# Optimization experiments

Measured on AMD Instinct MI355X. Metric: run time of the kernel, lower is better.

## Reference

```python
import math
import jax, jax.numpy as jnp
from jax import lax
import numpy as np

N, C, H, W = 32, 256, 56, 56

def setup_inputs() -> dict:
    key = jax.random.key(0)
    k = jax.random.split(key, 5)
    return {
        "x": jax.random.normal(k[0], (N, C, H, W), dtype=jnp.float32),
        "p1_w": jax.random.normal(k[1], (H, W, C, 1), dtype=jnp.float32) * 0.1,
        "conv_w": jax.random.normal(k[2], (C, C // 2, 3, 3), dtype=jnp.float32) * 0.05,
        "p4_w": jax.random.normal(k[3], (1, C, C), dtype=jnp.float32) * 0.1,
        "p5_w": jax.random.normal(k[4], (C, 1), dtype=jnp.float32) * 0.1,
    }

def reference(x, p1_w, conv_w, p4_w, p5_w):
    n, c, h, w = x.shape
    inv_sqrt_c = 1.0 / math.sqrt(c)
    # t_1: einsum 'abcd,cdef->abef' -> [n, c, c, 1] -> [n, c, c]
    t1 = jnp.einsum('nchw,hwef->ncef', x, p1_w)[..., 0]
    # t_3: grouped 3x3 conv, groups=2, no bias -> [n, c, h, w]
    t3 = lax.conv_general_dilated(
        x, conv_w, window_strides=(1, 1), padding=((1, 1), (1, 1)),
        dimension_numbers=('NCHW', 'OIHW', 'NCHW'), feature_group_count=2)
    # t_4: broadcast elementwise scale [1,c,c] * [n,c,c]
    t4 = p4_w * t1
    # t_5: [n,c,c] @ [c,1] -> [n,c]
    t5 = jnp.einsum('nab,bo->nao', t4, p5_w)[..., 0]
    # t_6: bmm(t4 [n,c,c], t3 [n,c,hw]) / sqrt(c) -> [n,c,h,w]
    t6 = (jnp.einsum('nab,nbs->nas', t4, t3.reshape(n, c, h * w))
          .reshape(n, c, h, w)) * inv_sqrt_c
    # t_7: bmm(t5 [n,1,c], x [n,c,hw]) / sqrt(c) -> [n,h,w]
    t7 = (jnp.einsum('nc,ncs->ns', t5, x.reshape(n, c, h * w))
          .reshape(n, h, w)) * inv_sqrt_c
    # t_8: broadcast add [n,1,h,w] + [n,c,h,w]
    return t7[:, None, :, :] + t6
```

## Files before the change

### kernel.cpp

```cpp
#include <hip/hip_runtime.h>

#define HWB   3136
#define HWPAD 3200
#define SPAD  3364

typedef __attribute__((ext_vector_type(8))) short bf16x8;
typedef __attribute__((ext_vector_type(4))) float f32x4;

__device__ __forceinline__ unsigned short f2bf(float f) {
    unsigned u = __float_as_uint(f);
    unsigned r = (u + 0x7fffu + ((u >> 16) & 1u)) >> 16;
    return (unsigned short)r;
}
__device__ __forceinline__ float bf2f(unsigned short h) {
    return __uint_as_float(((unsigned)h) << 16);
}
__device__ __forceinline__ void gl_lds16(const void* g, void* l) {
    __builtin_amdgcn_global_load_lds(
        (const __attribute__((address_space(1))) void*)g,
        (__attribute__((address_space(3))) void*)l, 16, 0, 0);
}

__global__ __launch_bounds__(256) void k_prep(
    const float* __restrict__ x, unsigned short* __restrict__ xc,
    unsigned short* __restrict__ xp,
    const float* __restrict__ p1, const float* __restrict__ cw,
    unsigned short* __restrict__ p1t, unsigned short* __restrict__ wp)
{
    const int b = blockIdx.x, t = threadIdx.x;
    if (b < 6272) {
        __shared__ unsigned tile[64 * 33];
        const int n = b / 196, rem = b - n * 196;
        const int c0 = (rem / 49) * 64, s0 = (rem % 49) * 64;
        const int cp = t >> 3;
        const int sg = (t & 7) * 8;

        const float* src = x + ((size_t)(n * 256 + c0 + 2 * cp)) * HWB + s0 + sg;
        unsigned short b0[8], b1[8];
        {
            float4 v0 = *(const float4*)(src);
            float4 v1 = *(const float4*)(src + 4);
            float4 w0 = *(const float4*)(src + HWB);
            float4 w1 = *(const float4*)(src + HWB + 4);
            b0[0] = f2bf(v0.x); b0[1] = f2bf(v0.y); b0[2] = f2bf(v0.z); b0[3] = f2bf(v0.w);
            b0[4] = f2bf(v1.x); b0[5] = f2bf(v1.y); b0[6] = f2bf(v1.z); b0[7] = f2bf(v1.w);
            b1[0] = f2bf(w0.x); b1[1] = f2bf(w0.y); b1[2] = f2bf(w0.z); b1[3] = f2bf(w0.w);
            b1[4] = f2bf(w1.x); b1[5] = f2bf(w1.y); b1[6] = f2bf(w1.z); b1[7] = f2bf(w1.w);
        }
        unsigned short* xcb = xc + ((size_t)(n * 256 + c0 + 2 * cp)) * HWB + s0 + sg;
        *(bf16x8*)xcb = *(const bf16x8*)&b0[0];
        *(bf16x8*)(xcb + HWB) = *(const bf16x8*)&b1[0];
#pragma unroll
        for (int k = 0; k < 8; ++k)
            tile[(sg + k) * 33 + cp] = (unsigned)b0[k] | ((unsigned)b1[k] << 16);
        __syncthreads();
        const int r = t >> 2;
        const int cq = (t & 3) * 8;
        unsigned d[8];
#pragma unroll
        for (int j = 0; j < 8; ++j)
            d[j] = tile[r * 33 + cq + j];
        const int s = s0 + r;
        const int sp = s + 2 * (s / 56) + 59;
        unsigned* dst = (unsigned*)(xp + ((size_t)n * SPAD + sp) * 256 + c0 + 2 * cq);
        *(uint4*)dst = make_uint4(d[0], d[1], d[2], d[3]);
        *(uint4*)(dst + 4) = make_uint4(d[4], d[5], d[6], d[7]);
    } else if (b < 7056) {
        __shared__ unsigned short tile[32][33];
        const int b2 = b - 6272;
        const int h0 = (b2 % 98) * 32, e0 = (b2 / 98) * 32;
        const int lx = t & 31, ly = t >> 5;
#pragma unroll
        for (int it = 0; it < 4; ++it) {
            int lh = ly + it * 8;
            tile[lh][lx] = f2bf(p1[(size_t)(h0 + lh) * 256 + e0 + lx]);
        }
        __syncthreads();
#pragma unroll
        for (int it = 0; it < 4; ++it) {
            int le = ly + it * 8;
            p1t[(size_t)(e0 + le) * HWB + h0 + lx] = tile[lx][le];
        }
    } else if (b < 7312) {
        const int o = b - 7056;
#pragma unroll
        for (int k = t; k < 1152; k += 256) {
            int tap = k >> 7, ci = k & 127;
            wp[(size_t)o * 1152 + k] = f2bf(cw[(size_t)o * 1152 + ci * 9 + tap]);
        }
    } else {
        const int bb = b - 7312;
        const int n = bb / 29, xb = bb - n * 29;
        const int idx = xb * 256 + t;
        if (idx < 228 * 32) {
            const int i = idx >> 5, ch = idx & 31;
            int sp;
            if (i < 58)       sp = i;
            else if (i < 116) sp = 3306 + (i - 58);
            else if (i < 172) sp = (i - 115) * 58;
            else              sp = (i - 171) * 58 + 57;
            bf16x8 z = {};
            *(bf16x8*)&xp[((size_t)n * SPAD + sp) * 256 + ch * 8] = z;
        }
    }
}

__global__ __launch_bounds__(256) void k_mfma(
    const unsigned short* __restrict__ xp, const unsigned short* __restrict__ wp,
    unsigned short* __restrict__ t3cl,
    const unsigned short* __restrict__ xc, const unsigned short* __restrict__ p1t,
    float* __restrict__ part)
{
    __shared__ short As[2][128 * 64];
    __shared__ short Bs[2][128 * 64];
    const int tid = threadIdx.x;
    const int wave = tid >> 6, lane = tid & 63;
    const int wm = (wave >> 1) * 64, wn = (wave & 1) * 64;
    const int rl = tid >> 3, q = tid & 7;
    const int swq = (q ^ (rl & 7)) * 8;
    const int ldst = rl * 64 + q * 8;
    const int frow = lane & 15, quad = lane >> 4, sw = frow & 7;

    if (blockIdx.x < 1600) {
        const int orig = blockIdx.x;
        const int wgid = (orig & 7) * 200 + (orig >> 3);
        const int ng = wgid / 25;
        const int tileS = (wgid - ng * 25) * 128;
        const int n = ng >> 1, g = ng & 1;

        const unsigned short* xpn = xp + (size_t)n * SPAD * 256 + g * 128 + swq;
        const unsigned short* arow[4];
        const unsigned short* brow[4];
#pragma unroll
        for (int p = 0; p < 4; ++p) {
            int s = tileS + p * 32 + rl;
            int sc = s < HWB ? s : HWB - 1;
            int sp = sc + 2 * (sc / 56) + 59;
            arow[p] = xpn + (size_t)sp * 256;
            brow[p] = wp + (size_t)(g * 128 + p * 32 + rl) * 1152 + swq;
        }

        f32x4 acc[4][4] = {};
        int rofA[4], rofB[4];
#pragma unroll
        for (int i = 0; i < 4; ++i) {
            rofA[i] = (wm + i * 16 + frow) * 64;
            rofB[i] = (wn + i * 16 + frow) * 64;
        }
        {
            const int shift0 = (-59) * 256;
#pragma unroll
            for (int p = 0; p < 4; ++p) {
                gl_lds16(arow[p] + shift0, &As[0][p * 2048 + ldst]);
                gl_lds16(brow[p], &Bs[0][p * 2048 + ldst]);
            }
        }
        __syncthreads();

        int cur = 0;
#pragma unroll
        for (int t = 0; t < 18; ++t) {
            if (t < 17) {
                const int tn = t + 1;
                const int tap = tn >> 1;
                const int shift = ((tap / 3 - 1) * 58 + (tap % 3 - 1)) * 256 + (tn & 1) * 64;
#pragma unroll
                for (int p = 0; p < 4; ++p) {
                    gl_lds16(arow[p] + shift, &As[cur ^ 1][p * 2048 + ldst]);
                    gl_lds16(brow[p] + tn * 64, &Bs[cur ^ 1][p * 2048 + ldst]);
                }
            }
            const short* Ab = As[cur];
            const short* Bb = Bs[cur];
#pragma unroll
            for (int h = 0; h < 2; ++h) {
                bf16x8 af[4], bfr[4];
#pragma unroll
                for (int i = 0; i < 4; ++i)
                    af[i] = *(const bf16x8*)&Ab[rofA[i] + ((h * 4 + quad) ^ sw) * 8];
#pragma unroll
                for (int j = 0; j < 4; ++j)
                    bfr[j] = *(const bf16x8*)&Bb[rofB[j] + ((h * 4 + quad) ^ sw) * 8];
#pragma unroll
                for (int i = 0; i < 4; ++i)
#pragma unroll
                    for (int j = 0; j < 4; ++j)
                        acc[i][j] = __builtin_amdgcn_mfma_f32_16x16x32_bf16(af[i], bfr[j], acc[i][j], 0, 0, 0);
            }
            __syncthreads();
            cur ^= 1;
        }
        unsigned short* ob = t3cl + (size_t)n * HWPAD * 256 + g * 128;
#pragma unroll
        for (int i = 0; i < 4; ++i)
#pragma unroll
            for (int r = 0; r < 4; ++r) {
                int s = tileS + wm + i * 16 + quad * 4 + r;
                int c = wn + frow;
#pragma unroll
                for (int j = 0; j < 4; ++j) {
                    float v = (s < HWB) ? acc[i][j][r] : 0.f;
                    ob[(size_t)s * 256 + c + j * 16] = f2bf(v);
                }
            }
    } else {
        const int orig = blockIdx.x - 1600;
        const int wgid = (orig & 7) * 32 + (orig >> 3);
        const int z = wgid >> 7;
        const int rem = wgid & 127;
        const int tileM = (rem >> 1) * 128;
        const int tileN = (rem & 1) * 128;
        const int kbase = z * 1600;
        const int nk = z ? 24 : 25;

        const unsigned short* asrc = xc + (size_t)(tileM + rl) * HWB + kbase + swq;
        const unsigned short* bsrc = p1t + (size_t)(tileN + rl) * HWB + kbase + swq;

        f32x4 acc[4][4] = {};
#pragma unroll
        for (int p = 0; p < 4; ++p) {
            gl_lds16(asrc + (size_t)(p * 32) * HWB, &As[0][p * 2048 + ldst]);
            gl_lds16(bsrc + (size_t)(p * 32) * HWB, &Bs[0][p * 2048 + ldst]);
        }
        __syncthreads();

        int cur = 0;
        for (int i2 = 0; i2 < nk; ++i2) {
            if (i2 + 1 < nk) {
                const int kn = (i2 + 1) * 64;
#pragma unroll
                for (int p = 0; p < 4; ++p) {
                    gl_lds16(asrc + (size_t)(p * 32) * HWB + kn, &As[cur ^ 1][p * 2048 + ldst]);
                    gl_lds16(bsrc + (size_t)(p * 32) * HWB + kn, &Bs[cur ^ 1][p * 2048 + ldst]);
                }
            }
            const short* Ab = As[cur];
            const short* Bb = Bs[cur];
#pragma unroll
            for (int h = 0; h < 2; ++h) {
                bf16x8 af[4], bfr[4];
#pragma unroll
                for (int i = 0; i < 4; ++i)
                    af[i] = *(const bf16x8*)&Ab[(wm + i * 16 + frow) * 64 + ((h * 4 + quad) ^ sw) * 8];
#pragma unroll
                for (int j = 0; j < 4; ++j)
                    bfr[j] = *(const bf16x8*)&Bb[(wn + j * 16 + frow) * 64 + ((h * 4 + quad) ^ sw) * 8];
#pragma unroll
                for (int i = 0; i < 4; ++i)
#pragma unroll
                    for (int j = 0; j < 4; ++j)
                        acc[i][j] = __builtin_amdgcn_mfma_f32_16x16x32_bf16(af[i], bfr[j], acc[i][j], 0, 0, 0);
            }
            __syncthreads();
            cur ^= 1;
        }
        float* ob = part + (size_t)z * 8192 * 256;
#pragma unroll
        for (int j = 0; j < 4; ++j) {
            const int e = tileN + wn + j * 16 + frow;
#pragma unroll
            for (int i = 0; i < 4; ++i)
#pragma unroll
                for (int r = 0; r < 4; ++r) {
                    int m = tileM + wm + i * 16 + quad * 4 + r;
                    ob[(size_t)m * 256 + e] = acc[i][j][r];
                }
        }
    }
}

__global__ __launch_bounds__(256) void k_t4scale(
    const float* __restrict__ part, const float* __restrict__ p4,
    const float* __restrict__ p5, unsigned short* __restrict__ t4h,
    float* __restrict__ t5)
{
    const int row = blockIdx.x * 4 + (threadIdx.x >> 6);
    const int lane = threadIdx.x & 63;
    const size_t off = (size_t)row * 256 + lane * 4;
    const size_t slab = (size_t)8192 * 256;
    float4 a0 = *(const float4*)&part[off];
    float4 a1 = *(const float4*)&part[off + slab];
    float4 a;
    a.x = a0.x + a1.x; a.y = a0.y + a1.y; a.z = a0.z + a1.z; a.w = a0.w + a1.w;
    float4 sc = *(const float4*)&p4[(size_t)(row & 255) * 256 + lane * 4];
    float4 pv = *(const float4*)&p5[lane * 4];
    float v0 = a.x * sc.x, v1 = a.y * sc.y, v2 = a.z * sc.z, v3 = a.w * sc.w;
    ushort4 o;
    o.x = f2bf(v0); o.y = f2bf(v1); o.z = f2bf(v2); o.w = f2bf(v3);
    *(ushort4*)&t4h[(size_t)row * 256 + lane * 4] = o;
    float sum = v0 * pv.x + v1 * pv.y + v2 * pv.z + v3 * pv.w;
#pragma unroll
    for (int offd = 32; offd > 0; offd >>= 1) sum += __shfl_down(sum, offd);
    if (lane == 0) t5[row] = sum;
}

__global__ __launch_bounds__(256) void k_bmm(
    const unsigned short* __restrict__ t4h, const unsigned short* __restrict__ t3cl,
    const unsigned short* __restrict__ xp, const float* __restrict__ t5,
    float* __restrict__ out)
{
    __shared__ short As[2][128 * 64];
    __shared__ short Bs[2][128 * 64];
    __shared__ float t5s[256];
    __shared__ float t7loc[128];
    const int tid = threadIdx.x;
    const int orig = blockIdx.x;
    const int wgid = (orig & 7) * 200 + (orig >> 3);
    const int n = wgid / 50;
    const int rem = wgid - n * 50;
    const int tileA = (rem / 25) * 128;
    const int tileS = (rem % 25) * 128;
    const int wave = tid >> 6, lane = tid & 63;
    const int wm = (wave >> 1) * 64, wn = (wave & 1) * 64;

    const int rl = tid >> 3, q = tid & 7;
    const int swq = (q ^ (rl & 7)) * 8;
    const unsigned short* asrc = t4h + ((size_t)n * 256 + tileA + rl) * 256 + swq;
    const unsigned short* bsrc = t3cl + ((size_t)n * HWPAD + tileS + rl) * 256 + swq;

    f32x4 acc[4][4] = {};
    const int frow = lane & 15, quad = lane >> 4, sw = frow & 7;
    const int ldst = rl * 64 + q * 8;

    t5s[tid] = t5[n * 256 + tid];
#pragma unroll
    for (int p = 0; p < 4; ++p) {
        gl_lds16(asrc + (size_t)(p * 32) * 256, &As[0][p * 2048 + ldst]);
        gl_lds16(bsrc + (size_t)(p * 32) * 256, &Bs[0][p * 2048 + ldst]);
    }
    __syncthreads();

    if (tid < 128) {
        const int s = tileS + tid;
        float accv = 0.f;
        if (s < HWB) {
            const int sp = s + 2 * (s / 56) + 59;
            const unsigned short* row = xp + ((size_t)n * SPAD + sp) * 256;
#pragma unroll
            for (int j = 0; j < 32; ++j) {
                bf16x8 v = *(const bf16x8*)(row + j * 8);
#pragma unroll
                for (int k = 0; k < 8; ++k)
                    accv += t5s[j * 8 + k] * bf2f((unsigned short)v[k]);
            }
        }
        t7loc[tid] = accv * 0.0625f;
    }

    int cur = 0;
#pragma unroll
    for (int k0 = 0; k0 < 256; k0 += 64) {
        if (k0 < 192) {
            const int kn = k0 + 64;
#pragma unroll
            for (int p = 0; p < 4; ++p) {
                gl_lds16(asrc + (size_t)(p * 32) * 256 + kn, &As[cur ^ 1][p * 2048 + ldst]);
                gl_lds16(bsrc + (size_t)(p * 32) * 256 + kn, &Bs[cur ^ 1][p * 2048 + ldst]);
            }
        }
        const short* Ab = As[cur];
        const short* Bb = Bs[cur];
#pragma unroll
        for (int h = 0; h < 2; ++h) {
            bf16x8 af[4], bfr[4];
#pragma unroll
            for (int i = 0; i < 4; ++i)
                af[i] = *(const bf16x8*)&Ab[(wm + i * 16 + frow) * 64 + ((h * 4 + quad) ^ sw) * 8];
#pragma unroll
            for (int j = 0; j < 4; ++j)
                bfr[j] = *(const bf16x8*)&Bb[(wn + j * 16 + frow) * 64 + ((h * 4 + quad) ^ sw) * 8];
#pragma unroll
            for (int i = 0; i < 4; ++i)
#pragma unroll
                for (int j = 0; j < 4; ++j)
                    acc[i][j] = __builtin_amdgcn_mfma_f32_16x16x32_bf16(af[i], bfr[j], acc[i][j], 0, 0, 0);
        }
        __syncthreads();
        cur ^= 1;
    }
    float* ob = out + (size_t)n * 256 * HWB;
#pragma unroll
    for (int j = 0; j < 4; ++j) {
        const int sLoc = wn + j * 16 + frow;
        const int s = tileS + sLoc;
        if (s >= HWB) continue;
        const float t7v = t7loc[sLoc];
#pragma unroll
        for (int i = 0; i < 4; ++i)
#pragma unroll
            for (int r = 0; r < 4; ++r) {
                int a = tileA + wm + i * 16 + quad * 4 + r;
                ob[(size_t)a * HWB + s] = acc[i][j][r] * 0.0625f + t7v;
            }
    }
}

extern "C" void kernel_launch(void* const* d_in, const int* in_sizes, int n_in,
                              void* d_out, int out_size, void* d_ws, size_t ws_size,
                              hipStream_t stream) {
    const float* x  = (const float*)d_in[0];
    const float* p1 = (const float*)d_in[1];
    const float* cw = (const float*)d_in[2];
    const float* p4 = (const float*)d_in[3];
    const float* p5 = (const float*)d_in[4];

    char* w = (char*)d_ws;
    unsigned short* xp    = (unsigned short*)w;  w += (size_t)32 * SPAD * 256 * 2;
    unsigned short* t3cl  = (unsigned short*)w;  w += (size_t)32 * HWPAD * 256 * 2;
    unsigned short* p1t   = (unsigned short*)w;  w += (size_t)256 * HWB * 2;
    unsigned short* wpack = (unsigned short*)w;  w += (size_t)256 * 1152 * 2;
    unsigned short* t4h   = (unsigned short*)w;  w += (size_t)8192 * 256 * 2;
    float* t5             = (float*)w;           w += (size_t)8192 * 4;

    char* o = (char*)d_out;
    unsigned short* xc = (unsigned short*)o;
    float* part        = (float*)(o + (size_t)32 * 256 * HWB * 2);
    float* out = (float*)d_out;

    k_prep    <<<dim3(8240),  256, 0, stream>>>(x, xc, xp, p1, cw, p1t, wpack);
    k_mfma    <<<dim3(1856),  256, 0, stream>>>(xp, wpack, t3cl, xc, p1t, part);
    k_t4scale <<<dim3(2048),  256, 0, stream>>>(part, p4, p5, t4h, t5);
    k_bmm     <<<dim3(1600),  256, 0, stream>>>(t4h, t3cl, xp, t5, out);
}
```

Before: 329.9 us.

## Fuse grouped conv into bmm kernel, keeping t3 tile in LDS

The grouped 3x3 conv is moved out of the combined MFMA kernel and fused into the final bmm kernel. Each block computes a 64-pixel by 256-channel conv tile for both groups, packs it to bf16 in LDS, and immediately multiplies by t4 (read directly from global), so the t3 intermediate is never written to or read back from HBM. The gemm1 part becomes its own small 256-block kernel. In exchange the bmm stage has smaller spatial tiles, reads t4 fragments from global without LDS staging, and carries more register pressure, which may lower occupancy. The gemm1 kernel also no longer overlaps with the conv work.

```diff
diff --git a/kernel.cpp b/kernel.cpp
--- a/kernel.cpp
+++ b/kernel.cpp
@@ -1,7 +1,6 @@
 #include <hip/hip_runtime.h>
 
 #define HWB   3136
-#define HWPAD 3200
 #define SPAD  3364
 
 typedef __attribute__((ext_vector_type(8))) short bf16x8;
@@ -105,167 +104,81 @@
     }
 }
 
-__global__ __launch_bounds__(256) void k_mfma(
-    const unsigned short* __restrict__ xp, const unsigned short* __restrict__ wp,
-    unsigned short* __restrict__ t3cl,
+__global__ __launch_bounds__(256) void k_gemm1(
     const unsigned short* __restrict__ xc, const unsigned short* __restrict__ p1t,
     float* __restrict__ part)
 {
     __shared__ short As[2][128 * 64];
     __shared__ short Bs[2][128 * 64];
     const int tid = threadIdx.x;
+    const int orig = blockIdx.x;
+    const int wgid = (orig & 7) * 32 + (orig >> 3);
+    const int z = wgid >> 7;
+    const int rem = wgid & 127;
+    const int tileM = (rem >> 1) * 128;
+    const int tileN = (rem & 1) * 128;
+    const int kbase = z * 1600;
+    const int nk = z ? 24 : 25;
     const int wave = tid >> 6, lane = tid & 63;
     const int wm = (wave >> 1) * 64, wn = (wave & 1) * 64;
+
     const int rl = tid >> 3, q = tid & 7;
     const int swq = (q ^ (rl & 7)) * 8;
+    const unsigned short* asrc = xc + (size_t)(tileM + rl) * HWB + kbase + swq;
+    const unsigned short* bsrc = p1t + (size_t)(tileN + rl) * HWB + kbase + swq;
+
+    f32x4 acc[4][4] = {};
+    const int frow = lane & 15, quad = lane >> 4, sw = frow & 7;
     const int ldst = rl * 64 + q * 8;
-    const int frow = lane & 15, quad = lane >> 4, sw = frow & 7;
-
-    if (blockIdx.x < 1600) {
-        const int orig = blockIdx.x;
-        const int wgid = (orig & 7) * 200 + (orig >> 3);
-        const int ng = wgid / 25;
-        const int tileS = (wgid - ng * 25) * 128;
-        const int n = ng >> 1, g = ng & 1;
-
-        const unsigned short* xpn = xp + (size_t)n * SPAD * 256 + g * 128 + swq;
-        const unsigned short* arow[4];
-        const unsigned short* brow[4];
-#pragma unroll
-        for (int p = 0; p < 4; ++p) {
-            int s = tileS + p * 32 + rl;
-            int sc = s < HWB ? s : HWB - 1;
-            int sp = sc + 2 * (sc / 56) + 59;
-            arow[p] = xpn + (size_t)sp * 256;
-            brow[p] = wp + (size_t)(g * 128 + p * 32 + rl) * 1152 + swq;
-        }
-
-        f32x4 acc[4][4] = {};
-        int rofA[4], rofB[4];
-#pragma unroll
-        for (int i = 0; i < 4; ++i) {
-            rofA[i] = (wm + i * 16 + frow) * 64;
-            rofB[i] = (wn + i * 16 + frow) * 64;
-        }
-        {
-            const int shift0 = (-59) * 256;
+
+#pragma unroll
+    for (int p = 0; p < 4; ++p) {
+        gl_lds16(asrc + (size_t)(p * 32) * HWB, &As[0][p * 2048 + ldst]);
+        gl_lds16(bsrc + (size_t)(p * 32) * HWB, &Bs[0][p * 2048 + ldst]);
+    }
+    __syncthreads();
+
+    int cur = 0;
+    for (int i2 = 0; i2 < nk; ++i2) {
+        if (i2 + 1 < nk) {
+            const int kn = (i2 + 1) * 64;
 #pragma unroll
             for (int p = 0; p < 4; ++p) {
-                gl_lds16(arow[p] + shift0, &As[0][p * 2048 + ldst]);
-                gl_lds16(brow[p], &Bs[0][p * 2048 + ldst]);
-            }
+                gl_lds16(asrc + (size_t)(p * 32) * HWB + kn, &As[cur ^ 1][p * 2048 + ldst]);
+                gl_lds16(bsrc + (size_t)(p * 32) * HWB + kn, &Bs[cur ^ 1][p * 2048 + ldst]);
+            }
+        }
+        const short* Ab = As[cur];
+        const short* Bb = Bs[cur];
+#pragma unroll
+        for (int h = 0; h < 2; ++h) {
+            bf16x8 af[4], bfr[4];
+#pragma unroll
+            for (int i = 0; i < 4; ++i)
+                af[i] = *(const bf16x8*)&Ab[(wm + i * 16 + frow) * 64 + ((h * 4 + quad) ^ sw) * 8];
+#pragma unroll
+            for (int j = 0; j < 4; ++j)
+                bfr[j] = *(const bf16x8*)&Bb[(wn + j * 16 + frow) * 64 + ((h * 4 + quad) ^ sw) * 8];
+#pragma unroll
+            for (int i = 0; i < 4; ++i)
+#pragma unroll
+                for (int j = 0; j < 4; ++j)
+                    acc[i][j] = __builtin_amdgcn_mfma_f32_16x16x32_bf16(af[i], bfr[j], acc[i][j], 0, 0, 0);
         }
         __syncthreads();
-
-        int cur = 0;
-#pragma unroll
-        for (int t = 0; t < 18; ++t) {
-            if (t < 17) {
-                const int tn = t + 1;
-                const int tap = tn >> 1;
-                const int shift = ((tap / 3 - 1) * 58 + (tap % 3 - 1)) * 256 + (tn & 1) * 64;
-#pragma unroll
-                for (int p = 0; p < 4; ++p) {
-                    gl_lds16(arow[p] + shift, &As[cur ^ 1][p * 2048 + ldst]);
-                    gl_lds16(brow[p] + tn * 64, &Bs[cur ^ 1][p * 2048 + ldst]);
-                }
-            }
-            const short* Ab = As[cur];
-            const short* Bb = Bs[cur];
-#pragma unroll
-            for (int h = 0; h < 2; ++h) {
-                bf16x8 af[4], bfr[4];
-#pragma unroll
-                for (int i = 0; i < 4; ++i)
-                    af[i] = *(const bf16x8*)&Ab[rofA[i] + ((h * 4 + quad) ^ sw) * 8];
-#pragma unroll
-                for (int j = 0; j < 4; ++j)
-                    bfr[j] = *(const bf16x8*)&Bb[rofB[j] + ((h * 4 + quad) ^ sw) * 8];
-#pragma unroll
-                for (int i = 0; i < 4; ++i)
-#pragma unroll
-                    for (int j = 0; j < 4; ++j)
-                        acc[i][j] = __builtin_amdgcn_mfma_f32_16x16x32_bf16(af[i], bfr[j], acc[i][j], 0, 0, 0);
-            }
-            __syncthreads();
-            cur ^= 1;
-        }
-        unsigned short* ob = t3cl + (size_t)n * HWPAD * 256 + g * 128;
+        cur ^= 1;
+    }
+    float* ob = part + (size_t)z * 8192 * 256;
+#pragma unroll
+    for (int j = 0; j < 4; ++j) {
+        const int e = tileN + wn + j * 16 + frow;
 #pragma unroll
         for (int i = 0; i < 4; ++i)
 #pragma unroll
             for (int r = 0; r < 4; ++r) {
-                int s = tileS + wm + i * 16 + quad * 4 + r;
-                int c = wn + frow;
-#pragma unroll
-                for (int j = 0; j < 4; ++j) {
-                    float v = (s < HWB) ? acc[i][j][r] : 0.f;
-                    ob[(size_t)s * 256 + c + j * 16] = f2bf(v);
-                }
-            }
-    } else {
-        const int orig = blockIdx.x - 1600;
-        const int wgid = (orig & 7) * 32 + (orig >> 3);
-        const int z = wgid >> 7;
-        const int rem = wgid & 127;
-        const int tileM = (rem >> 1) * 128;
-        const int tileN = (rem & 1) * 128;
-        const int kbase = z * 1600;
-        const int nk = z ? 24 : 25;
-
-        const unsigned short* asrc = xc + (size_t)(tileM + rl) * HWB + kbase + swq;
-        const unsigned short* bsrc = p1t + (size_t)(tileN + rl) * HWB + kbase + swq;
-
-        f32x4 acc[4][4] = {};
-#pragma unroll
-        for (int p = 0; p < 4; ++p) {
-            gl_lds16(asrc + (size_t)(p * 32) * HWB, &As[0][p * 2048 + ldst]);
-            gl_lds16(bsrc + (size_t)(p * 32) * HWB, &Bs[0][p * 2048 + ldst]);
-        }
-        __syncthreads();
-
-        int cur = 0;
-        for (int i2 = 0; i2 < nk; ++i2) {
-            if (i2 + 1 < nk) {
-                const int kn = (i2 + 1) * 64;
-#pragma unroll
-                for (int p = 0; p < 4; ++p) {
-                    gl_lds16(asrc + (size_t)(p * 32) * HWB + kn, &As[cur ^ 1][p * 2048 + ldst]);
-                    gl_lds16(bsrc + (size_t)(p * 32) * HWB + kn, &Bs[cur ^ 1][p * 2048 + ldst]);
-                }
-            }
-            const short* Ab = As[cur];
-            const short* Bb = Bs[cur];
-#pragma unroll
-            for (int h = 0; h < 2; ++h) {
-                bf16x8 af[4], bfr[4];
-#pragma unroll
-                for (int i = 0; i < 4; ++i)
-                    af[i] = *(const bf16x8*)&Ab[(wm + i * 16 + frow) * 64 + ((h * 4 + quad) ^ sw) * 8];
-#pragma unroll
-                for (int j = 0; j < 4; ++j)
-                    bfr[j] = *(const bf16x8*)&Bb[(wn + j * 16 + frow) * 64 + ((h * 4 + quad) ^ sw) * 8];
-#pragma unroll
-                for (int i = 0; i < 4; ++i)
-#pragma unroll
-                    for (int j = 0; j < 4; ++j)
-                        acc[i][j] = __builtin_amdgcn_mfma_f32_16x16x32_bf16(af[i], bfr[j], acc[i][j], 0, 0, 0);
-            }
-            __syncthreads();
-            cur ^= 1;
-        }
-        float* ob = part + (size_t)z * 8192 * 256;
-#pragma unroll
-        for (int j = 0; j < 4; ++j) {
-            const int e = tileN + wn + j * 16 + frow;
-#pragma unroll
-            for (int i = 0; i < 4; ++i)
-#pragma unroll
-                for (int r = 0; r < 4; ++r) {
-                    int m = tileM + wm + i * 16 + quad * 4 + r;
-                    ob[(size_t)m * 256 + e] = acc[i][j][r];
-                }
-        }
+                int m = tileM + wm + i * 16 + quad * 4 + r;
+                ob[(size_t)m * 256 + e] = acc[i][j][r];
+            }
     }
 }
 
@@ -294,103 +207,174 @@
     if (lane == 0) t5[row] = sum;
 }
 
-__global__ __launch_bounds__(256) void k_bmm(
-    const unsigned short* __restrict__ t4h, const unsigned short* __restrict__ t3cl,
-    const unsigned short* __restrict__ xp, const float* __restrict__ t5,
+__global__ __launch_bounds__(256) void k_convbmm(
+    const unsigned short* __restrict__ xp, const unsigned short* __restrict__ wp,
+    const unsigned short* __restrict__ t4h, const float* __restrict__ t5,
     float* __restrict__ out)
 {
-    __shared__ short As[2][128 * 64];
-    __shared__ short Bs[2][128 * 64];
+    __shared__ short stg[24576];
     __shared__ float t5s[256];
-    __shared__ float t7loc[128];
+    __shared__ float t7loc[64];
     const int tid = threadIdx.x;
     const int orig = blockIdx.x;
-    const int wgid = (orig & 7) * 200 + (orig >> 3);
-    const int n = wgid / 50;
-    const int rem = wgid - n * 50;
-    const int tileA = (rem / 25) * 128;
-    const int tileS = (rem % 25) * 128;
+    const int wgid = (orig & 7) * 196 + (orig >> 3);
+    const int n = wgid / 49;
+    const int tileS = (wgid - n * 49) * 64;
     const int wave = tid >> 6, lane = tid & 63;
-    const int wm = (wave >> 1) * 64, wn = (wave & 1) * 64;
-
+    const int wm = (wave >> 1) * 32, wn = (wave & 1) * 64;
     const int rl = tid >> 3, q = tid & 7;
     const int swq = (q ^ (rl & 7)) * 8;
-    const unsigned short* asrc = t4h + ((size_t)n * 256 + tileA + rl) * 256 + swq;
-    const unsigned short* bsrc = t3cl + ((size_t)n * HWPAD + tileS + rl) * 256 + swq;
-
-    f32x4 acc[4][4] = {};
+    const int ldst = rl * 64 + q * 8;
     const int frow = lane & 15, quad = lane >> 4, sw = frow & 7;
-    const int ldst = rl * 64 + q * 8;
 
     t5s[tid] = t5[n * 256 + tid];
-#pragma unroll
-    for (int p = 0; p < 4; ++p) {
-        gl_lds16(asrc + (size_t)(p * 32) * 256, &As[0][p * 2048 + ldst]);
-        gl_lds16(bsrc + (size_t)(p * 32) * 256, &Bs[0][p * 2048 + ldst]);
+
+    int spA[2];
+#pragma unroll
+    for (int p = 0; p < 2; ++p) {
+        int s = tileS + p * 32 + rl;
+        spA[p] = s + 2 * (s / 56) + 59;
+    }
+
+    unsigned pk[2][4][2];
+    f32x4 acc[2][4];
+
+    for (int g = 0; g < 2; ++g) {
+        const unsigned short* xpn = xp + (size_t)n * SPAD * 256 + g * 128 + swq;
+        const unsigned short* arow[2];
+        const unsigned short* brow[4];
+#pragma unroll
+        for (int p = 0; p < 2; ++p) arow[p] = xpn + (size_t)spA[p] * 256;
+#pragma unroll
+        for (int p = 0; p < 4; ++p)
+            brow[p] = wp + (size_t)(g * 128 + p * 32 + rl) * 1152 + swq;
+#pragma unroll
+        for (int i = 0; i < 2; ++i)
+#pragma unroll
+            for (int j = 0; j < 4; ++j) acc[i][j] = (f32x4){0.f, 0.f, 0.f, 0.f};
+
+        {
+            const int shift0 = (-59) * 256;
+#pragma unroll
+            for (int p = 0; p < 2; ++p)
+                gl_lds16(arow[p] + shift0, &stg[p * 2048 + ldst]);
+#pragma unroll
+            for (int p = 0; p < 4; ++p)
+                gl_lds16(brow[p], &stg[8192 + p * 2048 + ldst]);
+        }
+        __syncthreads();
+
+        int cur = 0;
+#pragma unroll
+        for (int t = 0; t < 18; ++t) {
+            if (t < 17) {
+                const int tn = t + 1;
+                const int tap = tn >> 1;
+                const int shift = ((tap / 3 - 1) * 58 + (tap % 3 - 1)) * 256 + (tn & 1) * 64;
+#pragma unroll
+                for (int p = 0; p < 2; ++p)
+                    gl_lds16(arow[p] + shift, &stg[(cur ^ 1) * 4096 + p * 2048 + ldst]);
+#pragma unroll
+                for (int p = 0; p < 4; ++p)
+                    gl_lds16(brow[p] + tn * 64, &stg[8192 + (cur ^ 1) * 8192 + p * 2048 + ldst]);
+            }
+            const short* Ab = &stg[cur * 4096];
+            const short* Bb = &stg[8192 + cur * 8192];
+#pragma unroll
+            for (int h = 0; h < 2; ++h) {
+                bf16x8 af[2], bfr[4];
+#pragma unroll
+                for (int i = 0; i < 2; ++i)
+                    af[i] = *(const bf16x8*)&Ab[(wm + i * 16 + frow) * 64 + ((h * 4 + quad) ^ sw) * 8];
+#pragma unroll
+                for (int j = 0; j < 4; ++j)
+                    bfr[j] = *(const bf16x8*)&Bb[(wn + j * 16 + frow) * 64 + ((h * 4 + quad) ^ sw) * 8];
+#pragma unroll
+                for (int i = 0; i < 2; ++i)
+#pragma unroll
+                    for (int j = 0; j < 4; ++j)
+                        acc[i][j] = __builtin_amdgcn_mfma_f32_16x16x32_bf16(af[i], bfr[j], acc[i][j], 0, 0, 0);
+            }
+            __syncthreads();
+            cur ^= 1;
+        }
+        if (g == 0) {
+#pragma unroll
+            for (int i = 0; i < 2; ++i)
+#pragma unroll
+                for (int j = 0; j < 4; ++j) {
+                    pk[i][j][0] = (unsigned)f2bf(acc[i][j][0]) | ((unsigned)f2bf(acc[i][j][1]) << 16);
+                    pk[i][j][1] = (unsigned)f2bf(acc[i][j][2]) | ((unsigned)f2bf(acc[i][j][3]) << 16);
+                }
+        }
+    }
+
+#pragma unroll
+    for (int i = 0; i < 2; ++i)
+#pragma unroll
+        for (int r = 0; r < 4; ++r) {
+            const int sLoc = wm + i * 16 + quad * 4 + r;
+            const int key = sLoc & 7;
+#pragma unroll
+            for (int j = 0; j < 4; ++j) {
+                const int oc0 = wn + j * 16 + frow;
+                const unsigned short v0 = (unsigned short)(pk[i][j][r >> 1] >> ((r & 1) * 16));
+                stg[sLoc * 256 + (((oc0 >> 3) ^ key) << 3) + (oc0 & 7)] = (short)v0;
+                const int oc1 = 128 + oc0;
+                stg[sLoc * 256 + (((oc1 >> 3) ^ key) << 3) + (oc1 & 7)] = (short)f2bf(acc[i][j][r]);
+            }
+        }
+    if (tid < 64) {
+        const int s = tileS + tid;
+        const int sp = s + 2 * (s / 56) + 59;
+        const unsigned short* row = xp + ((size_t)n * SPAD + sp) * 256;
+        float accv = 0.f;
+#pragma unroll
+        for (int j = 0; j < 32; ++j) {
+            bf16x8 v = *(const bf16x8*)(row + j * 8);
+#pragma unroll
+            for (int k = 0; k < 8; ++k)
+                accv += t5s[j * 8 + k] * bf2f((unsigned short)v[k]);
+        }
+        t7loc[tid] = accv * 0.0625f;
     }
     __syncthreads();
 
-    if (tid < 128) {
-        const int s = tileS + tid;
-        float accv = 0.f;
-        if (s < HWB) {
-            const int sp = s + 2 * (s / 56) + 59;
-            const unsigned short* row = xp + ((size_t)n * SPAD + sp) * 256;
-#pragma unroll
-            for (int j = 0; j < 32; ++j) {
-                bf16x8 v = *(const bf16x8*)(row + j * 8);
-#pragma unroll
-                for (int k = 0; k < 8; ++k)
-                    accv += t5s[j * 8 + k] * bf2f((unsigned short)v[k]);
-            }
-        }
-        t7loc[tid] = accv * 0.0625f;
-    }
-
-    int cur = 0;
+    const int wm2 = wave * 64;
+    f32x4 acc2[4][4] = {};
+    const unsigned short* a2 = t4h + ((size_t)n * 256 + wm2 + frow) * 256;
 #pragma unroll
     for (int k0 = 0; k0 < 256; k0 += 64) {
-        if (k0 < 192) {
-            const int kn = k0 + 64;
-#pragma unroll
-            for (int p = 0; p < 4; ++p) {
-                gl_lds16(asrc + (size_t)(p * 32) * 256 + kn, &As[cur ^ 1][p * 2048 + ldst]);
-                gl_lds16(bsrc + (size_t)(p * 32) * 256 + kn, &Bs[cur ^ 1][p * 2048 + ldst]);
-            }
-        }
-        const short* Ab = As[cur];
-        const short* Bb = Bs[cur];
 #pragma unroll
         for (int h = 0; h < 2; ++h) {
+            const int kc8 = (k0 >> 3) + h * 4 + quad;
             bf16x8 af[4], bfr[4];
 #pragma unroll
             for (int i = 0; i < 4; ++i)
-                af[i] = *(const bf16x8*)&Ab[(wm + i * 16 + frow) * 64 + ((h * 4 + quad) ^ sw) * 8];
+                af[i] = *(const bf16x8*)&a2[(size_t)i * 16 * 256 + kc8 * 8];
 #pragma unroll
             for (int j = 0; j < 4; ++j)
-                bfr[j] = *(const bf16x8*)&Bb[(wn + j * 16 + frow) * 64 + ((h * 4 + quad) ^ sw) * 8];
+                bfr[j] = *(const bf16x8*)&stg[(j * 16 + frow) * 256 + ((kc8 ^ sw) << 3)];
 #pragma unroll
             for (int i = 0; i < 4; ++i)
 #pragma unroll
                 for (int j = 0; j < 4; ++j)
-                    acc[i][j] = __builtin_amdgcn_mfma_f32_16x16x32_bf16(af[i], bfr[j], acc[i][j], 0, 0, 0);
-        }
-        __syncthreads();
-        cur ^= 1;
-    }
+                    acc2[i][j] = __builtin_amdgcn_mfma_f32_16x16x32_bf16(af[i], bfr[j], acc2[i][j], 0, 0, 0);
+        }
+    }
+
     float* ob = out + (size_t)n * 256 * HWB;
 #pragma unroll
     for (int j = 0; j < 4; ++j) {
-        const int sLoc = wn + j * 16 + frow;
+        const int sLoc = j * 16 + frow;
         const int s = tileS + sLoc;
-        if (s >= HWB) continue;
         const float t7v = t7loc[sLoc];
 #pragma unroll
         for (int i = 0; i < 4; ++i)
 #pragma unroll
             for (int r = 0; r < 4; ++r) {
-                int a = tileA + wm + i * 16 + quad * 4 + r;
-                ob[(size_t)a * HWB + s] = acc[i][j][r] * 0.0625f + t7v;
+                const int a = wm2 + i * 16 + quad * 4 + r;
+                ob[(size_t)a * HWB + s] = acc2[i][j][r] * 0.0625f + t7v;
             }
     }
 }
@@ -406,7 +390,6 @@
 
     char* w = (char*)d_ws;
     unsigned short* xp    = (unsigned short*)w;  w += (size_t)32 * SPAD * 256 * 2;
-    unsigned short* t3cl  = (unsigned short*)w;  w += (size_t)32 * HWPAD * 256 * 2;
     unsigned short* p1t   = (unsigned short*)w;  w += (size_t)256 * HWB * 2;
     unsigned short* wpack = (unsigned short*)w;  w += (size_t)256 * 1152 * 2;
     unsigned short* t4h   = (unsigned short*)w;  w += (size_t)8192 * 256 * 2;
@@ -418,7 +401,7 @@
     float* out = (float*)d_out;
 
     k_prep    <<<dim3(8240),  256, 0, stream>>>(x, xc, xp, p1, cw, p1t, wpack);
-    k_mfma    <<<dim3(1856),  256, 0, stream>>>(xp, wpack, t3cl, xc, p1t, part);
+    k_gemm1   <<<dim3(256),   256, 0, stream>>>(xc, p1t, part);
     k_t4scale <<<dim3(2048),  256, 0, stream>>>(part, p4, p5, t4h, t5);
-    k_bmm     <<<dim3(1600),  256, 0, stream>>>(t4h, t3cl, xp, t5, out);
-}
+    k_convbmm <<<dim3(1568),  256, 0, stream>>>(xp, wpack, t4h, t5, out);
+}
```

Result: slower. 384.0 us (+16.4%).

## Fuse t4 scaling and t5 reduction into einsum GEMM epilogue, drop split-K

Applied to the files above, without the earlier changes.

The t1 GEMM blocks now run the full K range of 49 steps instead of splitting K in two. Their epilogue applies the p4 scale, writes t4 in bf16, and reduces t5 with shuffles plus atomicAdd. This removes the fp32 partial buffer round-trip and the separate k_t4scale launch. The einsum blocks are moved to the front of the grid so their longer tiles start early. The cost is 128 long-running blocks instead of 256 shorter ones, plus an extra memset and atomics on t5.

```diff
diff --git a/kernel.cpp b/kernel.cpp
--- a/kernel.cpp
+++ b/kernel.cpp
@@ -109,7 +109,8 @@
     const unsigned short* __restrict__ xp, const unsigned short* __restrict__ wp,
     unsigned short* __restrict__ t3cl,
     const unsigned short* __restrict__ xc, const unsigned short* __restrict__ p1t,
-    float* __restrict__ part)
+    const float* __restrict__ p4, const float* __restrict__ p5,
+    unsigned short* __restrict__ t4h, float* __restrict__ t5)
 {
     __shared__ short As[2][128 * 64];
     __shared__ short Bs[2][128 * 64];
@@ -121,8 +122,8 @@
     const int ldst = rl * 64 + q * 8;
     const int frow = lane & 15, quad = lane >> 4, sw = frow & 7;
 
-    if (blockIdx.x < 1600) {
-        const int orig = blockIdx.x;
+    if (blockIdx.x >= 128) {
+        const int orig = blockIdx.x - 128;
         const int wgid = (orig & 7) * 200 + (orig >> 3);
         const int ng = wgid / 25;
         const int tileS = (wgid - ng * 25) * 128;
@@ -204,17 +205,13 @@
                 }
             }
     } else {
-        const int orig = blockIdx.x - 1600;
-        const int wgid = (orig & 7) * 32 + (orig >> 3);
-        const int z = wgid >> 7;
-        const int rem = wgid & 127;
-        const int tileM = (rem >> 1) * 128;
-        const int tileN = (rem & 1) * 128;
-        const int kbase = z * 1600;
-        const int nk = z ? 24 : 25;
-
-        const unsigned short* asrc = xc + (size_t)(tileM + rl) * HWB + kbase + swq;
-        const unsigned short* bsrc = p1t + (size_t)(tileN + rl) * HWB + kbase + swq;
+        const int orig = blockIdx.x;
+        const int wgid = (orig & 7) * 16 + (orig >> 3);
+        const int tileM = (wgid >> 1) * 128;
+        const int tileN = (wgid & 1) * 128;
+
+        const unsigned short* asrc = xc + (size_t)(tileM + rl) * HWB + swq;
+        const unsigned short* bsrc = p1t + (size_t)(tileN + rl) * HWB + swq;
 
         f32x4 acc[4][4] = {};
 #pragma unroll
@@ -225,8 +222,8 @@
         __syncthreads();
 
         int cur = 0;
-        for (int i2 = 0; i2 < nk; ++i2) {
-            if (i2 + 1 < nk) {
+        for (int i2 = 0; i2 < 49; ++i2) {
+            if (i2 + 1 < 49) {
                 const int kn = (i2 + 1) * 64;
 #pragma unroll
                 for (int p = 0; p < 4; ++p) {
@@ -254,44 +251,30 @@
             __syncthreads();
             cur ^= 1;
         }
-        float* ob = part + (size_t)z * 8192 * 256;
-#pragma unroll
-        for (int j = 0; j < 4; ++j) {
-            const int e = tileN + wn + j * 16 + frow;
-#pragma unroll
-            for (int i = 0; i < 4; ++i)
-#pragma unroll
-                for (int r = 0; r < 4; ++r) {
-                    int m = tileM + wm + i * 16 + quad * 4 + r;
-                    ob[(size_t)m * 256 + e] = acc[i][j][r];
+        float p5v[4];
+#pragma unroll
+        for (int j = 0; j < 4; ++j)
+            p5v[j] = p5[tileN + wn + j * 16 + frow];
+#pragma unroll
+        for (int i = 0; i < 4; ++i)
+#pragma unroll
+            for (int r = 0; r < 4; ++r) {
+                const int m = tileM + wm + i * 16 + quad * 4 + r;
+                const float* p4row = p4 + (size_t)(m & 255) * 256;
+                float s = 0.f;
+#pragma unroll
+                for (int j = 0; j < 4; ++j) {
+                    const int e = tileN + wn + j * 16 + frow;
+                    const float t4v = acc[i][j][r] * p4row[e];
+                    t4h[(size_t)m * 256 + e] = f2bf(t4v);
+                    s += t4v * p5v[j];
                 }
-        }
-    }
-}
-
-__global__ __launch_bounds__(256) void k_t4scale(
-    const float* __restrict__ part, const float* __restrict__ p4,
-    const float* __restrict__ p5, unsigned short* __restrict__ t4h,
-    float* __restrict__ t5)
-{
-    const int row = blockIdx.x * 4 + (threadIdx.x >> 6);
-    const int lane = threadIdx.x & 63;
-    const size_t off = (size_t)row * 256 + lane * 4;
-    const size_t slab = (size_t)8192 * 256;
-    float4 a0 = *(const float4*)&part[off];
-    float4 a1 = *(const float4*)&part[off + slab];
-    float4 a;
-    a.x = a0.x + a1.x; a.y = a0.y + a1.y; a.z = a0.z + a1.z; a.w = a0.w + a1.w;
-    float4 sc = *(const float4*)&p4[(size_t)(row & 255) * 256 + lane * 4];
-    float4 pv = *(const float4*)&p5[lane * 4];
-    float v0 = a.x * sc.x, v1 = a.y * sc.y, v2 = a.z * sc.z, v3 = a.w * sc.w;
-    ushort4 o;
-    o.x = f2bf(v0); o.y = f2bf(v1); o.z = f2bf(v2); o.w = f2bf(v3);
-    *(ushort4*)&t4h[(size_t)row * 256 + lane * 4] = o;
-    float sum = v0 * pv.x + v1 * pv.y + v2 * pv.z + v3 * pv.w;
-#pragma unroll
-    for (int offd = 32; offd > 0; offd >>= 1) sum += __shfl_down(sum, offd);
-    if (lane == 0) t5[row] = sum;
+#pragma unroll
+                for (int off = 1; off < 16; off <<= 1)
+                    s += __shfl_xor(s, off);
+                if (frow == 0) atomicAdd(&t5[m], s);
+            }
+    }
 }
 
 __global__ __launch_bounds__(256) void k_bmm(
@@ -414,11 +397,10 @@
 
     char* o = (char*)d_out;
     unsigned short* xc = (unsigned short*)o;
-    float* part        = (float*)(o + (size_t)32 * 256 * HWB * 2);
     float* out = (float*)d_out;
 
-    k_prep    <<<dim3(8240),  256, 0, stream>>>(x, xc, xp, p1, cw, p1t, wpack);
-    k_mfma    <<<dim3(1856),  256, 0, stream>>>(xp, wpack, t3cl, xc, p1t, part);
-    k_t4scale <<<dim3(2048),  256, 0, stream>>>(part, p4, p5, t4h, t5);
-    k_bmm     <<<dim3(1600),  256, 0, stream>>>(t4h, t3cl, xp, t5, out);
-}
+    hipMemsetAsync(t5, 0, (size_t)8192 * 4, stream);
+    k_prep <<<dim3(8240), 256, 0, stream>>>(x, xc, xp, p1, cw, p1t, wpack);
+    k_mfma <<<dim3(1728), 256, 0, stream>>>(xp, wpack, t3cl, xc, p1t, p4, p5, t4h, t5);
+    k_bmm  <<<dim3(1600), 256, 0, stream>>>(t4h, t3cl, xp, t5, out);
+}
```

Result: faster. 322.3 us (-2.3%).
